# Performance work log

Measured on AMD Instinct MI355X. Metric: run time of the kernel, lower is better.

## Reference

```python
import jax, jax.numpy as jnp
import numpy as np

NUM_HEADS = 16
D_MODEL = 1024
D_QKV = 64


def _xavier(key, shape):
    # xavier normal over last two dims (fan_in = D_MODEL, fan_out = D_QKV)
    std = float(np.sqrt(2.0 / (shape[-2] + shape[-1])))
    return jax.random.normal(key, shape, dtype=jnp.float32) * std


def setup_inputs() -> dict:
    key = jax.random.key(0)
    ks = jax.random.split(key, 9)
    B, L = 4, 2048
    q = jax.random.normal(ks[0], (B, L, D_MODEL), dtype=jnp.float32)
    k = jax.random.normal(ks[1], (B, L, D_MODEL), dtype=jnp.float32)
    v = jax.random.normal(ks[2], (B, L, D_MODEL), dtype=jnp.float32)
    mask = jax.random.randint(ks[3], (B, L, L), 0, 2, dtype=jnp.int32)
    Wq = _xavier(ks[4], (NUM_HEADS, D_MODEL, D_QKV))
    Wk = _xavier(ks[5], (NUM_HEADS, D_MODEL, D_QKV))
    Wv = _xavier(ks[6], (NUM_HEADS, D_MODEL, D_QKV))
    lim = float(1.0 / np.sqrt(D_MODEL))
    Wo_w = jax.random.uniform(ks[7], (D_MODEL, D_MODEL), minval=-lim, maxval=lim, dtype=jnp.float32)
    Wo_b = jax.random.uniform(ks[8], (D_MODEL,), minval=-lim, maxval=lim, dtype=jnp.float32)
    return {"q": q, "k": k, "v": v, "mask": mask,
            "Wq": Wq, "Wk": Wk, "Wv": Wv, "Wo_w": Wo_w, "Wo_b": Wo_b}


def reference(q, k, v, mask, Wq, Wk, Wv, Wo_w, Wo_b):
    B, L, _ = q.shape
    query = jnp.einsum('blm,nmd->bnld', q, Wq)   # [B,H,L,Dq]
    key_ = jnp.einsum('blm,nmd->bnld', k, Wk)
    value = jnp.einsum('blm,nmd->bnld', v, Wv)
    scores = jnp.einsum('bnld,bnmd->bnlm', query, key_) / jnp.sqrt(
        jnp.asarray(D_QKV, dtype=query.dtype))          # [B,H,L,L]
    scores = jnp.where(mask[:, None, :, :] == 0, jnp.asarray(-1e9, scores.dtype), scores)
    attn = jax.nn.softmax(scores, axis=-1)
    out = jnp.einsum('bnlm,bnmd->bnld', attn, value)     # [B,H,L,Dq]
    out = out.transpose(0, 2, 1, 3).reshape(B, L, D_MODEL)
    return out @ Wo_w.T + Wo_b
```

## Files before the change

### kernel.cpp

```cpp
#include <hip/hip_runtime.h>
#include <stdint.h>

typedef __bf16 bf16;
typedef __bf16 bf16x8 __attribute__((ext_vector_type(8)));
typedef float  f32x4  __attribute__((ext_vector_type(4)));
typedef uint32_t u32;
typedef uint64_t u64;

#define SCALE_L2E 0.18033688011112042f

__device__ __forceinline__ void gld_lds16(const void* gsrc, void* ldst) {
  __builtin_amdgcn_global_load_lds(
      (const __attribute__((address_space(1))) void*)gsrc,
      (__attribute__((address_space(3))) void*)ldst, 16, 0, 0);
}

__global__ void prep(const float* __restrict__ q, const float* __restrict__ k,
                     const float* __restrict__ v, const int* __restrict__ mask,
                     const float* __restrict__ Wq, const float* __restrict__ Wk,
                     const float* __restrict__ Wv, const float* __restrict__ Wo,
                     bf16* __restrict__ qkv, bf16* __restrict__ Wt, u32* __restrict__ mbits) {
  const int z = blockIdx.z;
  const int tg = blockIdx.x * 256 + threadIdx.x;
  if (z < 3) {
    const float* in = (z == 0) ? q : (z == 1) ? k : v;
    bf16* o = qkv + (size_t)z * 8388608;
#pragma unroll
    for (int it = 0; it < 2; ++it) {
      int i = tg + it * 524288;
      const float4* p = (const float4*)(in + (size_t)i * 8);
      float4 a = p[0], b = p[1];
      bf16x8 vv;
      vv[0]=(bf16)a.x; vv[1]=(bf16)a.y; vv[2]=(bf16)a.z; vv[3]=(bf16)a.w;
      vv[4]=(bf16)b.x; vv[5]=(bf16)b.y; vv[6]=(bf16)b.z; vv[7]=(bf16)b.w;
      *(bf16x8*)(o + (size_t)i * 8) = vv;
    }
  } else if (z == 3) {
    int s = tg >> 17;
    int t = tg & 131071;
    int n = t >> 7, kb = t & 127;
    const float* W = (s == 0) ? Wq : (s == 1) ? Wk : (s == 2) ? Wv : Wo;
    bf16x8 vv;
    if (s < 3) {
#pragma unroll
      for (int j = 0; j < 8; ++j)
        vv[j] = (bf16)W[((n >> 6) << 16) + (kb * 8 + j) * 64 + (n & 63)];
    } else {
      const float4* p = (const float4*)&W[n * 1024 + kb * 8];
      float4 a = p[0], b = p[1];
      vv[0]=(bf16)a.x; vv[1]=(bf16)a.y; vv[2]=(bf16)a.z; vv[3]=(bf16)a.w;
      vv[4]=(bf16)b.x; vv[5]=(bf16)b.y; vv[6]=(bf16)b.z; vv[7]=(bf16)b.w;
    }
    *(bf16x8*)&Wt[(size_t)s * 1048576 + (size_t)n * 1024 + kb * 8] = vv;
  } else {
    for (int idx = tg; idx < 16777216; idx += 524288) {
      int m = mask[idx];
      u64 bal = __ballot(m != 0);
      if ((threadIdx.x & 63) == 0)
        *(u64*)&mbits[idx >> 5] = bal;
    }
  }
}


#define GEMM_CORE(Ap_, Bp_)                                                    \
  __shared__ bf16 sA[2][8192];                                                 \
  __shared__ bf16 sB[2][8192];                                                 \
  const int lane = threadIdx.x & 63, w = threadIdx.x >> 6;                     \
  const int c = lane & 15, g = lane >> 4;                                      \
  const int wr = w >> 1, wc = w & 1;                                           \
  const int c7 = c & 7;                                                        \
  const int ric = lane >> 3;                                                   \
  const int pblk = (lane & 7) ^ (ric & 7);                                     \
  const bf16* Asrc[4];                                                         \
  const bf16* Bsrc[4];                                                         \
  _Pragma("unroll")                                                            \
  for (int ii = 0; ii < 4; ++ii) {                                             \
    int r = 8 * (w * 4 + ii) + ric;                                            \
    Asrc[ii] = (Ap_) + (size_t)r * 1024 + pblk * 8;                            \
    Bsrc[ii] = (Bp_) + (size_t)r * 1024 + pblk * 8;                            \
  }                                                                            \
  const int y0 = (g ^ c7) << 4;                                                \
  const int y1 = ((4 + g) ^ c7) << 4;                                          \
  const int abase = wr * 8192 + c * 128;                                       \
  const int bbase = wc * 8192 + c * 128;                                       \
  f32x4 acc[4][4] = {};                                                        \
  _Pragma("unroll")                                                            \
  for (int ii = 0; ii < 4; ++ii) {                                             \
    gld_lds16(Asrc[ii], (char*)&sA[0][0] + (w * 4 + ii) * 1024);               \
    gld_lds16(Bsrc[ii], (char*)&sB[0][0] + (w * 4 + ii) * 1024);               \
  }                                                                            \
  for (int k0 = 0; k0 < 1024; k0 += 64) {                                      \
    __syncthreads();                                                           \
    int cb = (k0 >> 6) & 1, nb = cb ^ 1;                                       \
    if (k0 < 960) {                                                            \
      _Pragma("unroll")                                                        \
      for (int ii = 0; ii < 4; ++ii) {                                         \
        gld_lds16(Asrc[ii] + k0 + 64, (char*)&sA[nb][0] + (w * 4 + ii) * 1024);\
        gld_lds16(Bsrc[ii] + k0 + 64, (char*)&sB[nb][0] + (w * 4 + ii) * 1024);\
      }                                                                        \
    }                                                                          \
    const char* a8 = (const char*)&sA[cb][0] + abase;                          \
    const char* b8 = (const char*)&sB[cb][0] + bbase;                          \
    _Pragma("unroll")                                                          \
    for (int kk = 0; kk < 2; ++kk) {                                           \
      const int yk = kk ? y1 : y0;                                             \
      bf16x8 af[4], bfr[4];                                                    \
      _Pragma("unroll")                                                        \
      for (int m = 0; m < 4; ++m)                                              \
        af[m] = *(const bf16x8*)(a8 + m * 2048 + yk);                          \
      _Pragma("unroll")                                                        \
      for (int n = 0; n < 4; ++n)                                              \
        bfr[n] = *(const bf16x8*)(b8 + n * 2048 + yk);                         \
      _Pragma("unroll")                                                        \
      for (int m = 0; m < 4; ++m)                                              \
        _Pragma("unroll")                                                      \
        for (int n = 0; n < 4; ++n)                                            \
          acc[m][n] = __builtin_amdgcn_mfma_f32_16x16x32_bf16(af[m], bfr[n], acc[m][n], 0, 0, 0); \
    }                                                                          \
  }

__global__ __launch_bounds__(256, 2)
void proj_fused(const bf16* __restrict__ qkv, const bf16* __restrict__ Wt,
                bf16* __restrict__ Qp, bf16* __restrict__ Kp, bf16* __restrict__ Vt) {
  const int wg = blockIdx.x;
  const bf16* Ap;
  const bf16* Bp;
  int row0, col0, stage;
  if (wg < 1024) {
    int swz = (wg & 7) * 128 + (wg >> 3);
    int bx = swz & 7, by = swz >> 3;
    row0 = by * 128; col0 = bx * 128;
    stage = (row0 >= 8192) ? 1 : 0;
    Ap = qkv + (size_t)row0 * 1024;
    Bp = Wt + (stage ? 1048576 : 0) + (size_t)col0 * 1024;
  } else {
    int w2 = wg - 1024;
    int bz = w2 >> 7, rem = w2 & 127;
    int swz = (rem & 7) * 16 + (rem >> 3);
    int bx = swz & 15, by = swz >> 4;
    row0 = by * 128; col0 = bx * 128;
    stage = 2 + bz;
    Ap = Wt + 2097152 + (size_t)row0 * 1024;
    Bp = qkv + 16777216 + (size_t)bz * 2097152 + (size_t)col0 * 1024;
  }

  GEMM_CORE(Ap, Bp)

  if (stage <= 1) {
    float csc = stage ? 1.0f : SCALE_L2E;
    bf16* dst = stage ? Kp : Qp;
#pragma unroll
    for (int m = 0; m < 4; ++m) {
      int row_base = (row0 & 8191) + wr * 64 + m * 16 + g * 4;
#pragma unroll
      for (int n = 0; n < 4; ++n) {
        int col = col0 + wc * 64 + n * 16 + c;
#pragma unroll
        for (int r = 0; r < 4; ++r) {
          int row = row_base + r;
          int b = row >> 11, l = row & 2047, h = col >> 6, d = col & 63;
          dst[(((size_t)(b * 16 + h) * 2048 + l) << 6) + d] = (bf16)(acc[m][n][r] * csc);
        }
      }
    }
  } else {
    int bz = stage - 2;
#pragma unroll
    for (int m = 0; m < 4; ++m) {
      int row_base = row0 + wr * 64 + m * 16 + g * 4;
#pragma unroll
      for (int n = 0; n < 4; ++n) {
        int col = col0 + wc * 64 + n * 16 + c;
#pragma unroll
        for (int r = 0; r < 4; ++r)
          Vt[((size_t)(bz * 1024 + row_base + r)) * 2048 + col] = (bf16)acc[m][n][r];
      }
    }
  }
}

__global__ __launch_bounds__(256, 2)
void gemm_out(const bf16* __restrict__ X, const bf16* __restrict__ Wot,
              float* __restrict__ out, const float* __restrict__ bias) {
  int lin = blockIdx.y * 8 + blockIdx.x;
  int swz = (lin & 7) * 64 + (lin >> 3);
  int bx = swz & 7, by = swz >> 3;
  const int row0 = by * 128, col0 = bx * 128;
  const bf16* Ap = X + (size_t)row0 * 1024;
  const bf16* Bp = Wot + (size_t)col0 * 1024;

  GEMM_CORE(Ap, Bp)

#pragma unroll
  for (int m = 0; m < 4; ++m) {
    int row_base = row0 + wr * 64 + m * 16 + g * 4;
#pragma unroll
    for (int n = 0; n < 4; ++n) {
      int col = col0 + wc * 64 + n * 16 + c;
#pragma unroll
      for (int r = 0; r < 4; ++r)
        out[(size_t)(row_base + r) * 1024 + col] = acc[m][n][r] + bias[col];
    }
  }
}

__global__ __launch_bounds__(256, 4)
void attn_fwd(const bf16* __restrict__ Qp, const bf16* __restrict__ Kp,
              const bf16* __restrict__ Vt, const u32* __restrict__ mbits,
              bf16* __restrict__ X) {
  int lin = blockIdx.y * 16 + blockIdx.x;
  int swz = (lin & 7) * 128 + (lin >> 3);
  int qt = swz & 15, bh = swz >> 4;
  int b = bh >> 4, h = bh & 15;
  int q0 = qt * 128;

  const int tid = threadIdx.x;
  const int lane = tid & 63, w = tid >> 6;
  const int c = lane & 15, g = lane >> 4;

  __shared__ char smem[24576];
  char* sKV = smem;
  char* sPw = smem + 16384 + w * 2048;

  const int c7 = c & 7;
  const int ko0 = c * 128 + ((g ^ c7) << 4);
  const int ko1 = c * 128 + (((4 + g) ^ c7) << 4);
  const int pr_off = (c >> 1) * 128 + ((((c & 1) * 4 + g) ^ (c >> 1)) << 4);
  int pwo[2];
#pragma unroll
  for (int nk = 0; nk < 2; ++nk)
    pwo[nk] = (c >> 1) * 128 + ((((c & 1) * 4 + nk * 2 + (g >> 1)) ^ (c >> 1)) << 4) + (g & 1) * 8;

  const int kr_ = tid >> 3, kb_ = tid & 7;
  const int dK = kr_ * 128 + ((kb_ ^ (kr_ & 7)) << 4);
  const int vd_ = tid >> 2, vk_ = tid & 3;
  const int dV = 4096 + (vd_ >> 1) * 128 + (((((vd_ & 1) << 2) + vk_) ^ ((vd_ >> 1) & 7)) << 4);
  const bf16* gK = Kp + (size_t)bh * 131072 + kr_ * 64 + kb_ * 8;
  const bf16* gV = Vt + ((size_t)(b * 1024 + h * 64 + vd_)) * 2048 + vk_ * 8;

  const bf16* Qbase = Qp + ((size_t)bh * 2048) * 64;
  bf16x8 qf[2][2];
#pragma unroll
  for (int nq = 0; nq < 2; ++nq) {
    int qg = q0 + w * 32 + nq * 16 + c;
#pragma unroll
    for (int kk = 0; kk < 2; ++kk)
      qf[nq][kk] = *(const bf16x8*)&Qbase[(size_t)qg * 64 + kk * 32 + g * 8];
  }

  bf16x8 onesv;
#pragma unroll
  for (int i = 0; i < 8; ++i) onesv[i] = (bf16)1.0f;

  const u32* Mrow0 = mbits + ((size_t)b * 2048 + (q0 + w * 32 + c)) * 64;
  const u32* Mrow1 = mbits + ((size_t)b * 2048 + (q0 + w * 32 + 16 + c)) * 64;

  f32x4 oacc[4][2] = {};
  f32x4 dacc[2] = {};

  {
    uint4 kr = *(const uint4*)gK;
    uint4 vr = *(const uint4*)gV;
    *(uint4*)(sKV + dK) = kr;
    *(uint4*)(sKV + dV) = vr;
  }
  u32 mw0 = Mrow0[0], mw1 = Mrow1[0];

  for (int t = 0; t < 64; ++t) {
    __syncthreads();
    const char* kbuf = sKV + ((t & 1) << 13);

    uint4 kr, vr;
    u32 mn0 = 0, mn1 = 0;
    if (t < 63) {
      kr = *(const uint4*)(gK + (size_t)(t + 1) * 2048);
      vr = *(const uint4*)(gV + (size_t)(t + 1) * 32);
      mn0 = Mrow0[t + 1];
      mn1 = Mrow1[t + 1];
    }

    f32x4 st[2][2] = {};
    __builtin_amdgcn_s_setprio(1);
#pragma unroll
    for (int nk = 0; nk < 2; ++nk) {
      bf16x8 kfa = *(const bf16x8*)(kbuf + ko0 + nk * 2048);
      st[nk][0] = __builtin_amdgcn_mfma_f32_16x16x32_bf16(kfa, qf[0][0], st[nk][0], 0, 0, 0);
      st[nk][1] = __builtin_amdgcn_mfma_f32_16x16x32_bf16(kfa, qf[1][0], st[nk][1], 0, 0, 0);
      bf16x8 kfb = *(const bf16x8*)(kbuf + ko1 + nk * 2048);
      st[nk][0] = __builtin_amdgcn_mfma_f32_16x16x32_bf16(kfb, qf[0][1], st[nk][0], 0, 0, 0);
      st[nk][1] = __builtin_amdgcn_mfma_f32_16x16x32_bf16(kfb, qf[1][1], st[nk][1], 0, 0, 0);
    }
    __builtin_amdgcn_s_setprio(0);

#pragma unroll
    for (int nq = 0; nq < 2; ++nq) {
      u32 ms = (nq ? mw1 : mw0) >> (4 * g);
#pragma unroll
      for (int nk = 0; nk < 2; ++nk) {
        const int bs = nk * 16;
        float e0 = __builtin_amdgcn_exp2f(st[nk][nq][0]);
        float e1 = __builtin_amdgcn_exp2f(st[nk][nq][1]);
        float e2 = __builtin_amdgcn_exp2f(st[nk][nq][2]);
        float e3 = __builtin_amdgcn_exp2f(st[nk][nq][3]);
        e0 = (ms & (1u << (bs + 0))) ? e0 : 0.f;
        e1 = (ms & (1u << (bs + 1))) ? e1 : 0.f;
        e2 = (ms & (1u << (bs + 2))) ? e2 : 0.f;
        e3 = (ms & (1u << (bs + 3))) ? e3 : 0.f;
        union { bf16 hh[4]; uint2 dd; } pk;
        pk.hh[0] = (bf16)e0; pk.hh[1] = (bf16)e1;
        pk.hh[2] = (bf16)e2; pk.hh[3] = (bf16)e3;
        *(uint2*)(sPw + pwo[nk] + nq * 1024) = pk.dd;
      }
    }

    __builtin_amdgcn_s_setprio(1);
    {
      bf16x8 pf0 = *(const bf16x8*)(sPw + pr_off);
      bf16x8 pf1 = *(const bf16x8*)(sPw + pr_off + 1024);
      dacc[0] = __builtin_amdgcn_mfma_f32_16x16x32_bf16(onesv, pf0, dacc[0], 0, 0, 0);
      dacc[1] = __builtin_amdgcn_mfma_f32_16x16x32_bf16(onesv, pf1, dacc[1], 0, 0, 0);
#pragma unroll
      for (int md = 0; md < 4; ++md) {
        bf16x8 vf = *(const bf16x8*)(kbuf + 4096 + pr_off + md * 1024);
        oacc[md][0] = __builtin_amdgcn_mfma_f32_16x16x32_bf16(vf, pf0, oacc[md][0], 0, 0, 0);
        oacc[md][1] = __builtin_amdgcn_mfma_f32_16x16x32_bf16(vf, pf1, oacc[md][1], 0, 0, 0);
      }
    }
    __builtin_amdgcn_s_setprio(0);

    if (t < 63) {
      char* nbuf = sKV + (((t + 1) & 1) << 13);
      *(uint4*)(nbuf + dK) = kr;
      *(uint4*)(nbuf + dV) = vr;
    }
    mw0 = mn0; mw1 = mn1;
  }

  float inv0 = 1.f / dacc[0][0];
  float inv1 = 1.f / dacc[1][0];

  __syncthreads();
  char* Xl = smem;
#pragma unroll
  for (int nq = 0; nq < 2; ++nq) {
    float inv = nq ? inv1 : inv0;
    int ql = w * 32 + nq * 16 + c;
#pragma unroll
    for (int md = 0; md < 4; ++md)
#pragma unroll
      for (int r = 0; r < 4; ++r) {
        int d = md * 16 + g * 4 + r;
        int blk = d >> 3, off = d & 7;
        *(bf16*)(Xl + ql * 128 + ((blk ^ (ql & 7)) << 4) + off * 2) =
            (bf16)(oacc[md][nq][r] * inv);
      }
  }
  __syncthreads();
#pragma unroll
  for (int i = 0; i < 4; ++i) {
    int u = i * 256 + tid;
    int row = u >> 3, blk = u & 7;
    uint4 xv = *(const uint4*)(Xl + row * 128 + ((blk ^ (row & 7)) << 4));
    *(uint4*)&X[(size_t)(b * 2048 + q0 + row) * 1024 + h * 64 + blk * 8] = xv;
  }
}


extern "C" void kernel_launch(void* const* d_in, const int* in_sizes, int n_in,
                              void* d_out, int out_size, void* d_ws, size_t ws_size,
                              hipStream_t stream) {
  const float* q    = (const float*)d_in[0];
  const float* k    = (const float*)d_in[1];
  const float* v    = (const float*)d_in[2];
  const int*   mask = (const int*)d_in[3];
  const float* Wq   = (const float*)d_in[4];
  const float* Wk   = (const float*)d_in[5];
  const float* Wv   = (const float*)d_in[6];
  const float* Wo   = (const float*)d_in[7];
  const float* Wb   = (const float*)d_in[8];

  char* ws = (char*)d_ws;
  bf16* qkv = (bf16*)(ws + 0);
  bf16* Wt  = (bf16*)(ws + 50331648);
  bf16* Qp  = (bf16*)(ws + 58720256);
  bf16* Kp  = (bf16*)(ws + 75497472);
  bf16* Vt  = (bf16*)(ws + 92274688);
  bf16* Xb  = (bf16*)(ws + 109051904);
  u32*  mb  = (u32*) (ws + 125829120);

  prep<<<dim3(2048, 1, 5), 256, 0, stream>>>(q, k, v, mask, Wq, Wk, Wv, Wo, qkv, Wt, mb);

  proj_fused<<<dim3(1536, 1, 1), 256, 0, stream>>>(qkv, Wt, Qp, Kp, Vt);

  attn_fwd<<<dim3(16, 64, 1), 256, 0, stream>>>(Qp, Kp, Vt, mb, Xb);

  gemm_out<<<dim3(8, 64, 1), 256, 0, stream>>>(Xb, Wt + 3145728, (float*)d_out, Wb);
}
```

Measured before the change: 261.5 us.

## Halve GEMM K-tile to 32 with new swizzle, raise occupancy, LDS-transpose weight prep

The shared GEMM core now stages K-slices of 32 instead of 64, which halves LDS use per block. It uses a new XOR swizzle so each thread issues two direct-to-LDS loads per operand, and launch bounds go from 2 to 4 blocks per CU. The aim is more waves in flight to hide latency, at the cost of twice as many barriers per K loop. Separately, the Wq/Wk/Wv transpose-and-convert in prep now goes through an LDS tile so global reads are coalesced instead of strided.

```diff
diff --git a/kernel.cpp b/kernel.cpp
--- a/kernel.cpp
+++ b/kernel.cpp
@@ -20,8 +20,10 @@
                      const float* __restrict__ Wq, const float* __restrict__ Wk,
                      const float* __restrict__ Wv, const float* __restrict__ Wo,
                      bf16* __restrict__ qkv, bf16* __restrict__ Wt, u32* __restrict__ mbits) {
+  __shared__ float lds[64][65];
   const int z = blockIdx.z;
-  const int tg = blockIdx.x * 256 + threadIdx.x;
+  const int t = threadIdx.x;
+  const int tg = blockIdx.x * 256 + t;
   if (z < 3) {
     const float* in = (z == 0) ? q : (z == 1) ? k : v;
     bf16* o = qkv + (size_t)z * 8388608;
@@ -36,91 +38,100 @@
       *(bf16x8*)(o + (size_t)i * 8) = vv;
     }
   } else if (z == 3) {
-    int s = tg >> 17;
-    int t = tg & 131071;
-    int n = t >> 7, kb = t & 127;
-    const float* W = (s == 0) ? Wq : (s == 1) ? Wk : (s == 2) ? Wv : Wo;
-    bf16x8 vv;
-    if (s < 3) {
-#pragma unroll
-      for (int j = 0; j < 8; ++j)
-        vv[j] = (bf16)W[((n >> 6) << 16) + (kb * 8 + j) * 64 + (n & 63)];
-    } else {
-      const float4* p = (const float4*)&W[n * 1024 + kb * 8];
-      float4 a = p[0], b = p[1];
-      vv[0]=(bf16)a.x; vv[1]=(bf16)a.y; vv[2]=(bf16)a.z; vv[3]=(bf16)a.w;
-      vv[4]=(bf16)b.x; vv[5]=(bf16)b.y; vv[6]=(bf16)b.z; vv[7]=(bf16)b.w;
-    }
-    *(bf16x8*)&Wt[(size_t)s * 1048576 + (size_t)n * 1024 + kb * 8] = vv;
+    const int blk = blockIdx.x;
+    if (blk < 768) {
+      int s = blk >> 8, sub = blk & 255;
+      int h = sub >> 4, mblk = sub & 15;
+      const float* W = (s == 0) ? Wq : (s == 1) ? Wk : Wv;
+      const float* src = W + h * 65536 + mblk * 4096;
+#pragma unroll
+      for (int i = 0; i < 16; ++i) {
+        int idx = t + i * 256;
+        lds[idx >> 6][idx & 63] = src[idx];
+      }
+      __syncthreads();
+      int d = t >> 2, o0 = t & 3;
+#pragma unroll
+      for (int oo = 0; oo < 2; ++oo) {
+        int o = o0 + oo * 4;
+        bf16x8 vv;
+#pragma unroll
+        for (int j = 0; j < 8; ++j)
+          vv[j] = (bf16)lds[o * 8 + j][d];
+        *(bf16x8*)&Wt[(size_t)s * 1048576 + (size_t)(h * 64 + d) * 1024 + mblk * 64 + o * 8] = vv;
+      }
+    } else if (blk < 832) {
+      int idx0 = (blk - 768) * 256 + t;
+      for (int i = idx0; i < 131072; i += 16384) {
+        const float4* p = (const float4*)&Wo[i * 8];
+        float4 a = p[0], b = p[1];
+        bf16x8 vv;
+        vv[0]=(bf16)a.x; vv[1]=(bf16)a.y; vv[2]=(bf16)a.z; vv[3]=(bf16)a.w;
+        vv[4]=(bf16)b.x; vv[5]=(bf16)b.y; vv[6]=(bf16)b.z; vv[7]=(bf16)b.w;
+        *(bf16x8*)&Wt[3145728 + (size_t)i * 8] = vv;
+      }
+    }
   } else {
     for (int idx = tg; idx < 16777216; idx += 524288) {
       int m = mask[idx];
       u64 bal = __ballot(m != 0);
-      if ((threadIdx.x & 63) == 0)
+      if ((t & 63) == 0)
         *(u64*)&mbits[idx >> 5] = bal;
     }
   }
 }
 
-
 #define GEMM_CORE(Ap_, Bp_)                                                    \
-  __shared__ bf16 sA[2][8192];                                                 \
-  __shared__ bf16 sB[2][8192];                                                 \
-  const int lane = threadIdx.x & 63, w = threadIdx.x >> 6;                     \
+  __shared__ bf16 sA[2][4096];                                                 \
+  __shared__ bf16 sB[2][4096];                                                 \
+  const int tid = threadIdx.x;                                                 \
+  const int lane = tid & 63, w = tid >> 6;                                     \
   const int c = lane & 15, g = lane >> 4;                                      \
   const int wr = w >> 1, wc = w & 1;                                           \
-  const int c7 = c & 7;                                                        \
-  const int ric = lane >> 3;                                                   \
-  const int pblk = (lane & 7) ^ (ric & 7);                                     \
-  const bf16* Asrc[4];                                                         \
-  const bf16* Bsrc[4];                                                         \
-  _Pragma("unroll")                                                            \
-  for (int ii = 0; ii < 4; ++ii) {                                             \
-    int r = 8 * (w * 4 + ii) + ric;                                            \
-    Asrc[ii] = (Ap_) + (size_t)r * 1024 + pblk * 8;                            \
-    Bsrc[ii] = (Bp_) + (size_t)r * 1024 + pblk * 8;                            \
-  }                                                                            \
-  const int y0 = (g ^ c7) << 4;                                                \
-  const int y1 = ((4 + g) ^ c7) << 4;                                          \
-  const int abase = wr * 8192 + c * 128;                                       \
-  const int bbase = wc * 8192 + c * 128;                                       \
+  const int rr0 = tid >> 3, p0 = tid & 7;                                      \
+  const int l0 = p0 ^ (rr0 & 7);                                               \
+  const size_t so0 = (size_t)(2 * rr0 + (l0 >> 2)) * 1024 + (l0 & 3) * 8;      \
+  const int rr1 = (256 + tid) >> 3, p1 = tid & 7;                              \
+  const int l1 = p1 ^ (rr1 & 7);                                               \
+  const size_t so1 = (size_t)(2 * rr1 + (l1 >> 2)) * 1024 + (l1 & 3) * 8;      \
+  const bf16* As0 = (Ap_) + so0;                                               \
+  const bf16* As1 = (Ap_) + so1;                                               \
+  const bf16* Bs0 = (Bp_) + so0;                                               \
+  const bf16* Bs1 = (Bp_) + so1;                                               \
+  const int fro = (c >> 1) * 128 + ((((c & 1) * 4 + g) ^ (c >> 1)) << 4);      \
+  const int abase = wr * 4096 + fro;                                           \
+  const int bbase = wc * 4096 + fro;                                           \
   f32x4 acc[4][4] = {};                                                        \
-  _Pragma("unroll")                                                            \
-  for (int ii = 0; ii < 4; ++ii) {                                             \
-    gld_lds16(Asrc[ii], (char*)&sA[0][0] + (w * 4 + ii) * 1024);               \
-    gld_lds16(Bsrc[ii], (char*)&sB[0][0] + (w * 4 + ii) * 1024);               \
-  }                                                                            \
-  for (int k0 = 0; k0 < 1024; k0 += 64) {                                      \
+  gld_lds16(As0, (char*)&sA[0][0] + tid * 16);                                 \
+  gld_lds16(As1, (char*)&sA[0][0] + 4096 + tid * 16);                          \
+  gld_lds16(Bs0, (char*)&sB[0][0] + tid * 16);                                 \
+  gld_lds16(Bs1, (char*)&sB[0][0] + 4096 + tid * 16);                          \
+  for (int k0 = 0; k0 < 1024; k0 += 32) {                                      \
     __syncthreads();                                                           \
-    int cb = (k0 >> 6) & 1, nb = cb ^ 1;                                       \
-    if (k0 < 960) {                                                            \
-      _Pragma("unroll")                                                        \
-      for (int ii = 0; ii < 4; ++ii) {                                         \
-        gld_lds16(Asrc[ii] + k0 + 64, (char*)&sA[nb][0] + (w * 4 + ii) * 1024);\
-        gld_lds16(Bsrc[ii] + k0 + 64, (char*)&sB[nb][0] + (w * 4 + ii) * 1024);\
-      }                                                                        \
+    int cb = (k0 >> 5) & 1, nb = cb ^ 1;                                       \
+    if (k0 < 992) {                                                            \
+      gld_lds16(As0 + k0 + 32, (char*)&sA[nb][0] + tid * 16);                  \
+      gld_lds16(As1 + k0 + 32, (char*)&sA[nb][0] + 4096 + tid * 16);           \
+      gld_lds16(Bs0 + k0 + 32, (char*)&sB[nb][0] + tid * 16);                  \
+      gld_lds16(Bs1 + k0 + 32, (char*)&sB[nb][0] + 4096 + tid * 16);           \
     }                                                                          \
     const char* a8 = (const char*)&sA[cb][0] + abase;                          \
     const char* b8 = (const char*)&sB[cb][0] + bbase;                          \
+    bf16x8 af[4], bfr[4];                                                      \
     _Pragma("unroll")                                                          \
-    for (int kk = 0; kk < 2; ++kk) {                                           \
-      const int yk = kk ? y1 : y0;                                             \
-      bf16x8 af[4], bfr[4];                                                    \
-      _Pragma("unroll")                                                        \
-      for (int m = 0; m < 4; ++m)                                              \
-        af[m] = *(const bf16x8*)(a8 + m * 2048 + yk);                          \
+    for (int m = 0; m < 4; ++m)                                                \
+      af[m] = *(const bf16x8*)(a8 + m * 1024);                                 \
+    _Pragma("unroll")                                                          \
+    for (int n = 0; n < 4; ++n)                                                \
+      bfr[n] = *(const bf16x8*)(b8 + n * 1024);                                \
+    _Pragma("unroll")                                                          \
+    for (int m = 0; m < 4; ++m)                                                \
       _Pragma("unroll")                                                        \
       for (int n = 0; n < 4; ++n)                                              \
-        bfr[n] = *(const bf16x8*)(b8 + n * 2048 + yk);                         \
-      _Pragma("unroll")                                                        \
-      for (int m = 0; m < 4; ++m)                                              \
-        _Pragma("unroll")                                                      \
-        for (int n = 0; n < 4; ++n)                                            \
-          acc[m][n] = __builtin_amdgcn_mfma_f32_16x16x32_bf16(af[m], bfr[n], acc[m][n], 0, 0, 0); \
-    }                                                                          \
-  }
-
-__global__ __launch_bounds__(256, 2)
+        acc[m][n] = __builtin_amdgcn_mfma_f32_16x16x32_bf16(af[m], bfr[n], acc[m][n], 0, 0, 0); \
+  }
+
+__global__ __launch_bounds__(256, 4)
 void proj_fused(const bf16* __restrict__ qkv, const bf16* __restrict__ Wt,
                 bf16* __restrict__ Qp, bf16* __restrict__ Kp, bf16* __restrict__ Vt) {
   const int wg = blockIdx.x;
@@ -180,7 +191,7 @@
   }
 }
 
-__global__ __launch_bounds__(256, 2)
+__global__ __launch_bounds__(256, 4)
 void gemm_out(const bf16* __restrict__ X, const bf16* __restrict__ Wot,
               float* __restrict__ out, const float* __restrict__ bias) {
   int lin = blockIdx.y * 8 + blockIdx.x;
```

Measured after the change: 247.5 us. 5.3% less time.
